# Kernel optimization log

Measured on AMD Instinct MI355X. Metric: run time of the kernel, lower is better.

## Reference

```python
import jax, jax.numpy as jnp
import numpy as np

MODEL_DIM = 256
NUM_HEADS = 4
HEAD_DIM = MODEL_DIM // NUM_HEADS
MAX_LEN = 512
EPS = 1e-5


def positional_embedding(n, dim):
    pos = jnp.arange(n, dtype=jnp.float32)[:, None]
    div = jnp.exp(jnp.arange(0, dim, 2, dtype=jnp.float32) * (-np.log(10000.0) / dim))
    pe = jnp.zeros((n, dim), dtype=jnp.float32)
    pe = pe.at[:, 0::2].set(jnp.sin(pos * div))
    pe = pe.at[:, 1::2].set(jnp.cos(pos * div))
    return pe


def layer_norm(x, g, b):
    mu = jnp.mean(x, axis=-1, keepdims=True)
    var = jnp.mean(jnp.square(x - mu), axis=-1, keepdims=True)
    return (x - mu) * jax.lax.rsqrt(var + EPS) * g + b


def setup_inputs() -> dict:
    key = jax.random.key(0)
    ks = jax.random.split(key, 20)
    B, N = 64, 512
    d = MODEL_DIM

    def lin(k, fan_in, fan_out):
        lim = 1.0 / np.sqrt(fan_in)
        return jax.random.uniform(k, (fan_out, fan_in), jnp.float32, -lim, lim)

    def xavier(k, fan_in, fan_out):
        lim = np.sqrt(6.0 / (fan_in + fan_out))
        return jax.random.uniform(k, (fan_out, fan_in), jnp.float32, -lim, lim)

    return {
        "x": jax.random.normal(ks[0], (B, N, 769), jnp.float32),
        "y": jax.random.normal(ks[1], (B, N, 674), jnp.float32),
        "z": jnp.zeros((B, 1), jnp.float32),
        "Wr": lin(ks[2], 769, d), "br": jnp.zeros((d,), jnp.float32),
        "Wf": lin(ks[3], 674, d), "bf": jnp.zeros((d,), jnp.float32),
        "g_x": jnp.ones((d,), jnp.float32), "b_x": jnp.zeros((d,), jnp.float32),
        "g_y": jnp.ones((d,), jnp.float32), "b_y": jnp.zeros((d,), jnp.float32),
        "Wq": xavier(ks[4], d, d), "bq": jnp.zeros((d,), jnp.float32),
        "Wk": xavier(ks[5], d, d), "bk": jnp.zeros((d,), jnp.float32),
        "Wv": xavier(ks[6], d, d), "bv": jnp.zeros((d,), jnp.float32),
        "Wo": xavier(ks[7], d, d), "bo": jnp.zeros((d,), jnp.float32),
        "g_m": jnp.ones((d,), jnp.float32), "b_m": jnp.zeros((d,), jnp.float32),
        "W1": lin(ks[8], d, d), "b1": jnp.zeros((d,), jnp.float32),
        "W2": lin(ks[9], d, d), "b2": jnp.zeros((d,), jnp.float32),
        "Wc": lin(ks[10], d, 2), "bc": jnp.zeros((2,), jnp.float32),
    }


def reference(x, y, z, Wr, br, Wf, bf, g_x, b_x, g_y, b_y,
              Wq, bq, Wk, bk, Wv, bv, Wo, bo, g_m, b_m,
              W1, b1, W2, b2, Wc, bc):
    B, N, _ = x.shape
    d, H, hd = MODEL_DIM, NUM_HEADS, HEAD_DIM
    pe = positional_embedding(MAX_LEN, d)[:N]  # (N, d)

    xp = layer_norm(x @ Wr.T + br + pe[None], g_x, b_x)  # (B,N,d)
    yp = layer_norm(y @ Wf.T + bf + pe[None], g_y, b_y)

    # cross-attention (non-causal, no masks, eval-mode dropout)
    q = (xp @ Wq.T + bq).reshape(B, N, H, hd)
    k = (yp @ Wk.T + bk).reshape(B, N, H, hd)
    v = (yp @ Wv.T + bv).reshape(B, N, H, hd)
    scale = hd ** -0.5
    scores = jnp.einsum("bshd,bthd->bhst", q, k) * scale  # (B,H,N,N)
    attn = jax.nn.softmax(scores, axis=-1)
    ctx = jnp.einsum("bhst,bthd->bshd", attn, v).reshape(B, N, d)
    attn_out = ctx @ Wo.T + bo

    x_res = layer_norm(xp + attn_out, g_m, b_m)
    mlp = jax.nn.relu(x_res @ W1.T + b1) @ W2.T + b2
    x_mlp = x_res + mlp
    pooled = jnp.mean(x_mlp, axis=1)  # (B,d)
    logits = pooled @ Wc.T + bc  # (B,2)
    return logits
```

## Files before the change

kernel.cpp:

```cpp
#include <hip/hip_runtime.h>
#include <hip/hip_bf16.h>

#define B_   64
#define N_   512
#define D_   256
#define H_   4
#define HD_  64

typedef __hip_bfloat16 bf16;
typedef __attribute__((ext_vector_type(8))) short short8;
typedef __attribute__((ext_vector_type(4))) float floatx4;

__device__ __forceinline__ float bf2f(bf16 v) { return __bfloat162float(v); }
__device__ __forceinline__ unsigned short f2us(float f) {
    bf16 h = __float2bfloat16(f);
    union { bf16 h; unsigned short u; } c; c.h = h; return c.u;
}

typedef __attribute__((address_space(1))) const unsigned int asg_u32;
typedef __attribute__((address_space(3))) unsigned int asl_u32;
__device__ __forceinline__ void gl_lds16(const void* g, void* l) {
    __builtin_amdgcn_global_load_lds((asg_u32*)g, (asl_u32*)l, 16, 0, 0);
}

__device__ __forceinline__ void wait_vm12() { asm volatile("s_waitcnt vmcnt(12)" ::: "memory"); }
__device__ __forceinline__ void wait_vm5()  { asm volatile("s_waitcnt vmcnt(5)"  ::: "memory"); }
__device__ __forceinline__ void wait_vm0()  { asm volatile("s_waitcnt vmcnt(0)"  ::: "memory"); }
__device__ __forceinline__ void wait_lg0()  { asm volatile("s_waitcnt lgkmcnt(0)" ::: "memory"); }
__device__ __forceinline__ void bar()       { __builtin_amdgcn_s_barrier(); }
__device__ __forceinline__ void schedb()    { __builtin_amdgcn_sched_barrier(0); }

__global__ __launch_bounds__(256)
void convw_k(const float* __restrict__ Wr, const float* __restrict__ Wf,
             const float* __restrict__ Wq, const float* __restrict__ Wk,
             const float* __restrict__ Wv, const float* __restrict__ Wo,
             const float* __restrict__ W1, const float* __restrict__ W2,
             bf16* __restrict__ dst)
{
    const int seg = blockIdx.y;
    const float* src; int Kreal, Kp; size_t off;
    switch (seg) {
        case 0: src = Wr; Kreal = 769; Kp = 800; off = 0; break;
        case 1: src = Wf; Kreal = 674; Kp = 704; off = 256 * 800; break;
        default:
            src = (seg == 2) ? Wq : (seg == 3) ? Wk : (seg == 4) ? Wv
                : (seg == 5) ? Wo : (seg == 6) ? W1 : W2;
            Kreal = 256; Kp = 256;
            off = 256 * 800 + 256 * 704 + (size_t)(seg - 2) * 256 * 256;
            break;
    }
    const int idx = blockIdx.x * 256 + threadIdx.x;
    if (idx >= 256 * Kp / 8) return;
    const int rowk = idx * 8;
    const int n = rowk / Kp, k0 = rowk % Kp;
    unsigned short tmp[8];
    #pragma unroll
    for (int j = 0; j < 8; ++j) {
        int kk = k0 + j;
        tmp[j] = f2us(kk < Kreal ? src[(size_t)n * Kreal + kk] : 0.f);
    }
    *(short8*)&dst[off + (size_t)rowk] = *(short8*)tmp;
}

__global__ __launch_bounds__(256)
void pe_k(float* __restrict__ pe)
{
    const int n = blockIdx.x, c = threadIdx.x;
    const int j = c & ~1;
    float freq = __expf(-(float)j * (9.210340371976184f / 256.0f));
    float ang = (float)n * freq;
    pe[n * 256 + c] = (c & 1) ? cosf(ang) : sinf(ang);
}

template<bool F32A>
__global__ __launch_bounds__(256)
void gemm_rp_t(const bf16* __restrict__ A, const float* __restrict__ A32,
               int lda, int Kreal,
               const bf16* __restrict__ W, int ldw,
               const float* __restrict__ bias, const bf16* __restrict__ res,
               const float* __restrict__ pe,
               const float* __restrict__ g, const float* __restrict__ bln,
               bf16* __restrict__ C, float* __restrict__ pp,
               int Kp, int relu, int tv)
{
    __shared__ bf16 As[3][4 * 64 * 8];
    __shared__ bf16 Bs[3][4 * 256 * 8];
    __shared__ float s_mu[64][4], s_sq[64][4];

    const int tid = threadIdx.x;
    const int m0 = blockIdx.x * 64;
    const int lane = tid & 63, w = tid >> 6;
    const int fr = lane & 15, quad = lane >> 4;
    const int nt = Kp / 32;

    const unsigned short* Wp = (const unsigned short*)W + (size_t)lane * ldw + w * 8;

    floatx4 acc[4][4] = {};
    int rb = 0, w1 = 1, w2 = 2;

    if constexpr (F32A) {
        const int srow = tid >> 2, skb = tid & 3, kb8 = skb * 8;
        const float* a32p = A32 + (size_t)(m0 + srow) * Kreal + kb8;
        float avA[8], avB[8];

        #pragma unroll
        for (int j = 0; j < 8; ++j) avA[j] = a32p[j];
        #pragma unroll
        for (int i = 0; i < 4; ++i)
            gl_lds16(Wp + (size_t)(i * 64) * ldw, &Bs[0][(w * 256 + i * 64 + lane) * 8]);
        {
            unsigned short uw[8];
            #pragma unroll
            for (int j = 0; j < 8; ++j) uw[j] = f2us(avA[j]);
            *(short8*)&As[0][(skb * 64 + srow) * 8] = *(short8*)uw;
        }
        #pragma unroll
        for (int j = 0; j < 8; ++j) avB[j] = a32p[32 + j];
        #pragma unroll
        for (int i = 0; i < 4; ++i)
            gl_lds16(Wp + (size_t)(i * 64) * ldw + 32, &Bs[1][(w * 256 + i * 64 + lane) * 8]);

        auto f32a_step = [&](int t_, float (&AVC)[8], float (&AVN)[8]) {
            if (t_ + 1 < nt) { wait_vm12(); } else { wait_vm0(); }
            wait_lg0();
            bar();
            schedb();
            if (t_ + 2 < nt) {
                const int kL = (t_ + 2) * 32;
                if (kL + 32 <= Kreal) {
                    #pragma unroll
                    for (int j = 0; j < 8; ++j) AVN[j] = a32p[kL + j];
                } else {
                    #pragma unroll
                    for (int j = 0; j < 8; ++j) {
                        int kk = kL + kb8 + j;
                        int offv = (kk < Kreal) ? (kL + j) : 0;
                        float tvv = a32p[offv];
                        AVN[j] = (kk < Kreal) ? tvv : 0.f;
                    }
                }
                #pragma unroll
                for (int i = 0; i < 4; ++i)
                    gl_lds16(Wp + (size_t)(i * 64) * ldw + kL,
                             &Bs[w2][(w * 256 + i * 64 + lane) * 8]);
            }
            if (t_ + 1 < nt) {
                unsigned short uw[8];
                #pragma unroll
                for (int j = 0; j < 8; ++j) uw[j] = f2us(AVC[j]);
                *(short8*)&As[w1][(skb * 64 + srow) * 8] = *(short8*)uw;
            }
            schedb();
            short8 a[4];
            #pragma unroll
            for (int im = 0; im < 4; ++im)
                a[im] = *(const short8*)&As[rb][(quad * 64 + im * 16 + fr) * 8];
            #pragma unroll
            for (int in = 0; in < 4; ++in) {
                short8 bfrag = *(const short8*)&Bs[rb][(quad * 256 + w * 64 + in * 16 + fr) * 8];
                #pragma unroll
                for (int im = 0; im < 4; ++im)
                    acc[im][in] = __builtin_amdgcn_mfma_f32_16x16x32_bf16(
                        a[im], bfrag, acc[im][in], 0, 0, 0);
            }
            int tmp_ = rb; rb = w1; w1 = w2; w2 = tmp_;
        };
        for (int t = 0; t < nt; t += 2) {
            f32a_step(t, avB, avA);
            if (t + 1 < nt) f32a_step(t + 1, avA, avB);
        }
    } else {
        const unsigned short* Ap = (const unsigned short*)A + (size_t)(m0 + lane) * lda + w * 8;

        gl_lds16(Ap, &As[0][(w * 64 + lane) * 8]);
        #pragma unroll
        for (int i = 0; i < 4; ++i)
            gl_lds16(Wp + (size_t)(i * 64) * ldw, &Bs[0][(w * 256 + i * 64 + lane) * 8]);
        gl_lds16(Ap + 32, &As[1][(w * 64 + lane) * 8]);
        #pragma unroll
        for (int i = 0; i < 4; ++i)
            gl_lds16(Wp + (size_t)(i * 64) * ldw + 32, &Bs[1][(w * 256 + i * 64 + lane) * 8]);

        for (int t = 0; t < nt; ++t) {
            if (t + 1 < nt) { wait_vm5(); } else { wait_vm0(); }
            bar();
            schedb();
            if (t + 2 < nt) {
                const int kB = (t + 2) * 32;
                gl_lds16(Ap + kB, &As[w2][(w * 64 + lane) * 8]);
                #pragma unroll
                for (int i = 0; i < 4; ++i)
                    gl_lds16(Wp + (size_t)(i * 64) * ldw + kB,
                             &Bs[w2][(w * 256 + i * 64 + lane) * 8]);
            }
            schedb();
            short8 a[4];
            #pragma unroll
            for (int im = 0; im < 4; ++im)
                a[im] = *(const short8*)&As[rb][(quad * 64 + im * 16 + fr) * 8];
            #pragma unroll
            for (int in = 0; in < 4; ++in) {
                short8 bfrag = *(const short8*)&Bs[rb][(quad * 256 + w * 64 + in * 16 + fr) * 8];
                #pragma unroll
                for (int im = 0; im < 4; ++im)
                    acc[im][in] = __builtin_amdgcn_mfma_f32_16x16x32_bf16(
                        a[im], bfrag, acc[im][in], 0, 0, 0);
            }
            int tmp_ = rb; rb = w1; w1 = w2; w2 = tmp_;
        }
    }

    #pragma unroll
    for (int in = 0; in < 4; ++in) {
        const int n = w * 64 + in * 16 + fr;
        const float bi = bias[n];
        #pragma unroll
        for (int im = 0; im < 4; ++im) {
            #pragma unroll
            for (int reg = 0; reg < 4; ++reg) {
                const int m = m0 + im * 16 + quad * 4 + reg;
                float v = acc[im][in][reg] + bi;
                if (pe)   v += pe[((m & (N_ - 1)) << 8) + n];
                if (relu) v = fmaxf(v, 0.f);
                if (res)  v += bf2f(res[((size_t)m << 8) + n]);
                acc[im][in][reg] = v;
            }
        }
    }

    if (g) {
        #pragma unroll
        for (int im = 0; im < 4; ++im) {
            #pragma unroll
            for (int reg = 0; reg < 4; ++reg) {
                float ps = acc[im][0][reg] + acc[im][1][reg]
                         + acc[im][2][reg] + acc[im][3][reg];
                float pq = acc[im][0][reg] * acc[im][0][reg]
                         + acc[im][1][reg] * acc[im][1][reg]
                         + acc[im][2][reg] * acc[im][2][reg]
                         + acc[im][3][reg] * acc[im][3][reg];
                #pragma unroll
                for (int off = 1; off < 16; off <<= 1) {
                    ps += __shfl_xor(ps, off, 64);
                    pq += __shfl_xor(pq, off, 64);
                }
                if (fr == 0) {
                    const int r = im * 16 + quad * 4 + reg;
                    s_mu[r][w] = ps;
                    s_sq[r][w] = pq;
                }
            }
        }
        __syncthreads();
        #pragma unroll
        for (int im = 0; im < 4; ++im) {
            #pragma unroll
            for (int reg = 0; reg < 4; ++reg) {
                const int r = im * 16 + quad * 4 + reg;
                const float mu = (s_mu[r][0] + s_mu[r][1] + s_mu[r][2] + s_mu[r][3])
                                 * (1.f / 256.f);
                const float var = (s_sq[r][0] + s_sq[r][1] + s_sq[r][2] + s_sq[r][3])
                                  * (1.f / 256.f) - mu * mu;
                const float rs = rsqrtf(var + 1e-5f);
                const int m = m0 + r;
                #pragma unroll
                for (int in = 0; in < 4; ++in) {
                    const int n = w * 64 + in * 16 + fr;
                    C[((size_t)m << 8) + n] = __float2bfloat16(
                        (acc[im][in][reg] - mu) * rs * g[n] + bln[n]);
                }
            }
        }
    } else if (tv) {
        const int bh = ((m0 >> 9) << 2) + w;
        const int nn = m0 & (N_ - 1);
        unsigned short* Ct = (unsigned short*)C;
        #pragma unroll
        for (int in = 0; in < 4; ++in) {
            const int d = in * 16 + fr;
            #pragma unroll
            for (int im = 0; im < 4; ++im) {
                unsigned short pk[4];
                #pragma unroll
                for (int reg = 0; reg < 4; ++reg) pk[reg] = f2us(acc[im][in][reg]);
                *(ushort4*)&Ct[((size_t)(bh * 64 + d) << 9) + nn + im * 16 + quad * 4]
                    = *(ushort4*)pk;
            }
        }
    } else {
        #pragma unroll
        for (int im = 0; im < 4; ++im) {
            #pragma unroll
            for (int reg = 0; reg < 4; ++reg) {
                const int m = m0 + im * 16 + quad * 4 + reg;
                #pragma unroll
                for (int in = 0; in < 4; ++in) {
                    const int n = w * 64 + in * 16 + fr;
                    C[((size_t)m << 8) + n] = __float2bfloat16(acc[im][in][reg]);
                }
            }
        }
        if (pp) {
            #pragma unroll
            for (int in = 0; in < 4; ++in) {
                float s = 0.f;
                #pragma unroll
                for (int im = 0; im < 4; ++im)
                    #pragma unroll
                    for (int reg = 0; reg < 4; ++reg) s += acc[im][in][reg];
                s += __shfl_xor(s, 16, 64);
                s += __shfl_xor(s, 32, 64);
                if (quad == 0)
                    pp[((m0 >> 6) << 8) + w * 64 + in * 16 + fr] = s;
            }
        }
    }
}

__global__ __launch_bounds__(256)
void attn_k(const bf16* q, const bf16* __restrict__ k,
            const bf16* __restrict__ vt, bf16* ctx)
{
    __shared__ bf16 Ks[8 * 64 * 8];
    __shared__ bf16 Vs[8 * 64 * 8];
    __shared__ bf16 Ps[4 * 16 * 72];

    const int bid = blockIdx.x;
    const int l = (bid & 7) * 256 + (bid >> 3);
    const int qt = l & 7;
    const int h  = (l >> 3) & 3;
    const int b  = l >> 5;
    const int q0 = qt * 64;
    const size_t base  = ((size_t)b * N_) * D_ + h * HD_;
    const size_t vbase = ((size_t)(b * H_ + h) * HD_) * N_;

    const int tid = threadIdx.x;
    const int lane = tid & 63;
    const int w = tid >> 6;
    const int fr = lane & 15, quad = lane >> 4;

    short8 aq[2];
    #pragma unroll
    for (int ks = 0; ks < 2; ++ks)
        aq[ks] = *(const short8*)((const unsigned short*)q + base
                   + (size_t)(q0 + w * 16 + fr) * D_ + (ks * 4 + quad) * 8);

    floatx4 O[4] = {};
    float mrun[4], lrun[4];
    #pragma unroll
    for (int r = 0; r < 4; ++r) { mrun[r] = -1e30f; lrun[r] = 0.f; }

    const int srow = tid >> 2, sc = tid & 3;
    const unsigned short* kp = (const unsigned short*)k + base + (size_t)srow * D_ + sc * 16;
    const unsigned short* vp = (const unsigned short*)vt + vbase + (size_t)srow * N_ + sc * 16;
    const float C1 = 0.125f * 1.44269504f;

    for (int kt = 0; kt < 8; ++kt) {
        __syncthreads();
        {
            const unsigned short* srck = kp + (size_t)(kt * 64) * D_;
            *(short8*)&Ks[((sc * 2 + 0) * 64 + srow) * 8] = *(const short8*)(srck);
            *(short8*)&Ks[((sc * 2 + 1) * 64 + srow) * 8] = *(const short8*)(srck + 8);
            const unsigned short* srcv = vp + kt * 64;
            *(short8*)&Vs[((sc * 2 + 0) * 64 + srow) * 8] = *(const short8*)(srcv);
            *(short8*)&Vs[((sc * 2 + 1) * 64 + srow) * 8] = *(const short8*)(srcv + 8);
        }
        __syncthreads();

        floatx4 S[4] = {};
        __builtin_amdgcn_s_setprio(1);
        #pragma unroll
        for (int in = 0; in < 4; ++in) {
            #pragma unroll
            for (int ks = 0; ks < 2; ++ks) {
                short8 bk = *(const short8*)&Ks[((ks * 4 + quad) * 64 + in * 16 + fr) * 8];
                S[in] = __builtin_amdgcn_mfma_f32_16x16x32_bf16(aq[ks], bk, S[in], 0, 0, 0);
            }
        }
        __builtin_amdgcn_s_setprio(0);

        #pragma unroll
        for (int r = 0; r < 4; ++r) {
            float mloc = fmaxf(fmaxf(S[0][r], S[1][r]), fmaxf(S[2][r], S[3][r]));
            #pragma unroll
            for (int off = 1; off < 16; off <<= 1) mloc = fmaxf(mloc, __shfl_xor(mloc, off, 64));
            float mnew = fmaxf(mrun[r], mloc);
            float mc = mnew * C1;
            float alpha = exp2f(mrun[r] * C1 - mc);
            float rs = 0.f;
            #pragma unroll
            for (int in = 0; in < 4; ++in) {
                float p = exp2f(S[in][r] * C1 - mc);
                S[in][r] = p;
                rs += p;
            }
            #pragma unroll
            for (int off = 1; off < 16; off <<= 1) rs += __shfl_xor(rs, off, 64);
            lrun[r] = lrun[r] * alpha + rs;
            mrun[r] = mnew;
            #pragma unroll
            for (int in = 0; in < 4; ++in) O[in][r] *= alpha;
        }

        #pragma unroll
        for (int in = 0; in < 4; ++in)
            #pragma unroll
            for (int r = 0; r < 4; ++r)
                Ps[(w * 16 + quad * 4 + r) * 72 + in * 16 + fr] = __float2bfloat16(S[in][r]);
        short8 pa[2];
        #pragma unroll
        for (int ks = 0; ks < 2; ++ks)
            pa[ks] = *(const short8*)&Ps[(w * 16 + fr) * 72 + ks * 32 + quad * 8];

        __builtin_amdgcn_s_setprio(1);
        #pragma unroll
        for (int in = 0; in < 4; ++in) {
            #pragma unroll
            for (int ks = 0; ks < 2; ++ks) {
                short8 bv = *(const short8*)&Vs[((ks * 4 + quad) * 64 + in * 16 + fr) * 8];
                O[in] = __builtin_amdgcn_mfma_f32_16x16x32_bf16(pa[ks], bv, O[in], 0, 0, 0);
            }
        }
        __builtin_amdgcn_s_setprio(0);
    }

    #pragma unroll
    for (int r = 0; r < 4; ++r) {
        const float inv = 1.f / lrun[r];
        const int row = q0 + w * 16 + quad * 4 + r;
        #pragma unroll
        for (int in = 0; in < 4; ++in)
            ctx[base + (size_t)row * D_ + in * 16 + fr] = __float2bfloat16(O[in][r] * inv);
    }
}

__global__ __launch_bounds__(256)
void logits_k(const float* __restrict__ partial, const float* __restrict__ Wc,
              const float* __restrict__ bc, float* __restrict__ out)
{
    __shared__ float pl[256];
    __shared__ float red[256];
    int b = blockIdx.x, c = threadIdx.x;
    float s = 0.f;
    for (int ch = 0; ch < 8; ++ch) s += partial[((size_t)b * 8 + ch) * D_ + c];
    pl[c] = s * (1.f / 512.f);
    __syncthreads();
    int o = c >> 7, cc = c & 127;
    red[c] = pl[cc] * Wc[o * 256 + cc] + pl[cc + 128] * Wc[o * 256 + cc + 128];
    __syncthreads();
    for (int st = 64; st > 0; st >>= 1) { if (cc < st) red[c] += red[c + st]; __syncthreads(); }
    if (cc == 0) out[b * 2 + o] = red[c] + bc[o];
}

extern "C" void kernel_launch(void* const* d_in, const int* in_sizes, int n_in,
                              void* d_out, int out_size, void* d_ws, size_t ws_size,
                              hipStream_t stream)
{
    const float* x   = (const float*)d_in[0];
    const float* y   = (const float*)d_in[1];
    const float* Wr  = (const float*)d_in[3];
    const float* br  = (const float*)d_in[4];
    const float* Wf  = (const float*)d_in[5];
    const float* bfv = (const float*)d_in[6];
    const float* gx  = (const float*)d_in[7];
    const float* bx  = (const float*)d_in[8];
    const float* gy  = (const float*)d_in[9];
    const float* by  = (const float*)d_in[10];
    const float* Wq  = (const float*)d_in[11];
    const float* bq  = (const float*)d_in[12];
    const float* Wk  = (const float*)d_in[13];
    const float* bk  = (const float*)d_in[14];
    const float* Wv  = (const float*)d_in[15];
    const float* bv  = (const float*)d_in[16];
    const float* Wo  = (const float*)d_in[17];
    const float* bo  = (const float*)d_in[18];
    const float* gm  = (const float*)d_in[19];
    const float* bm  = (const float*)d_in[20];
    const float* W1  = (const float*)d_in[21];
    const float* b1  = (const float*)d_in[22];
    const float* W2  = (const float*)d_in[23];
    const float* b2  = (const float*)d_in[24];
    const float* Wc  = (const float*)d_in[25];
    const float* bc  = (const float*)d_in[26];

    bf16* ws = (bf16*)d_ws;
    const size_t S = (size_t)B_ * N_ * D_;
    bf16*  wb   = ws;
    float* pe   = (float*)(ws + 778240);
    float* part = pe + 131072;
    bf16*  bA   = ws + 778240 + 4 * 131072;
    bf16*  bB   = bA + S;
    bf16*  bC   = bB + S;
    bf16*  bD   = bC + S;
    bf16*  bE   = bD + S;

    bf16* Wrb = wb;
    bf16* Wfb = wb + 256 * 800;
    bf16* Wqb = Wfb + 256 * 704;
    bf16* Wkb = Wqb + 65536;
    bf16* Wvb = Wkb + 65536;
    bf16* Wob = Wvb + 65536;
    bf16* W1b = Wob + 65536;
    bf16* W2b = W1b + 65536;

    const int M = B_ * N_;
    dim3 blk(256);
    dim3 grp(M / 64);

    pe_k<<<N_, blk, 0, stream>>>(pe);
    convw_k<<<dim3(100, 8), blk, 0, stream>>>(Wr, Wf, Wq, Wk, Wv, Wo, W1, W2, wb);

    gemm_rp_t<true><<<grp, blk, 0, stream>>>(nullptr, x, 0, 769, Wrb, 800,
        br, nullptr, pe, gx, bx, bA, nullptr, 800, 0, 0);
    gemm_rp_t<true><<<grp, blk, 0, stream>>>(nullptr, y, 0, 674, Wfb, 704,
        bfv, nullptr, pe, gy, by, bB, nullptr, 704, 0, 0);
    gemm_rp_t<false><<<grp, blk, 0, stream>>>(bA, nullptr, 256, 256, Wqb, 256,
        bq, nullptr, nullptr, nullptr, nullptr, bC, nullptr, 256, 0, 0);
    gemm_rp_t<false><<<grp, blk, 0, stream>>>(bB, nullptr, 256, 256, Wkb, 256,
        bk, nullptr, nullptr, nullptr, nullptr, bD, nullptr, 256, 0, 0);
    gemm_rp_t<false><<<grp, blk, 0, stream>>>(bB, nullptr, 256, 256, Wvb, 256,
        bv, nullptr, nullptr, nullptr, nullptr, bE, nullptr, 256, 0, 1);
    attn_k<<<B_ * H_ * 8, blk, 0, stream>>>(bC, bD, bE, bC);
    gemm_rp_t<false><<<grp, blk, 0, stream>>>(bC, nullptr, 256, 256, Wob, 256,
        bo, bA, nullptr, gm, bm, bD, nullptr, 256, 0, 0);
    gemm_rp_t<false><<<grp, blk, 0, stream>>>(bD, nullptr, 256, 256, W1b, 256,
        b1, nullptr, nullptr, nullptr, nullptr, bE, nullptr, 256, 1, 0);
    gemm_rp_t<false><<<grp, blk, 0, stream>>>(bE, nullptr, 256, 256, W2b, 256,
        b2, bD, nullptr, nullptr, nullptr, bB, part, 256, 0, 0);
    logits_k<<<B_, blk, 0, stream>>>(part, Wc, bc, (float*)d_out);
}
```

Baseline: 549.9 us.

## Fuse K/V projections into one kernel and W1/W2 MLP into one kernel

```diff
diff --git a/kernel.cpp b/kernel.cpp
--- a/kernel.cpp
+++ b/kernel.cpp
@@ -271,22 +271,6 @@
                 }
             }
         }
-    } else if (tv) {
-        const int bh = ((m0 >> 9) << 2) + w;
-        const int nn = m0 & (N_ - 1);
-        unsigned short* Ct = (unsigned short*)C;
-        #pragma unroll
-        for (int in = 0; in < 4; ++in) {
-            const int d = in * 16 + fr;
-            #pragma unroll
-            for (int im = 0; im < 4; ++im) {
-                unsigned short pk[4];
-                #pragma unroll
-                for (int reg = 0; reg < 4; ++reg) pk[reg] = f2us(acc[im][in][reg]);
-                *(ushort4*)&Ct[((size_t)(bh * 64 + d) << 9) + nn + im * 16 + quad * 4]
-                    = *(ushort4*)pk;
-            }
-        }
     } else {
         #pragma unroll
         for (int im = 0; im < 4; ++im) {
@@ -300,19 +284,187 @@
                 }
             }
         }
-        if (pp) {
-            #pragma unroll
-            for (int in = 0; in < 4; ++in) {
-                float s = 0.f;
+    }
+}
+
+__global__ __launch_bounds__(512, 4)
+void kv_k(const bf16* __restrict__ A,
+          const bf16* __restrict__ Wk, const bf16* __restrict__ Wv,
+          const float* __restrict__ bk, const float* __restrict__ bv,
+          bf16* __restrict__ K, bf16* __restrict__ Vt)
+{
+    const int tid = threadIdx.x;
+    const int m0 = blockIdx.x * 64;
+    const int lane = tid & 63, w = tid >> 6;
+    const int isv = w >> 2;
+    const int cq = w & 3;
+    const int fr = lane & 15, quad = lane >> 4;
+
+    const unsigned short* wp = (const unsigned short*)(isv ? Wv : Wk)
+        + (size_t)(cq * 64 + fr) * 256 + quad * 8;
+    const unsigned short* ap = (const unsigned short*)A
+        + (size_t)(m0 + fr) * 256 + quad * 8;
+
+    floatx4 acc[4][4] = {};
+    for (int t = 0; t < 8; ++t) {
+        const int k0 = t * 32;
+        short8 fa[4], fb[4];
+        #pragma unroll
+        for (int i = 0; i < 4; ++i) {
+            fa[i] = *(const short8*)(ap + (size_t)(i * 16) * 256 + k0);
+            fb[i] = *(const short8*)(wp + (size_t)(i * 16) * 256 + k0);
+        }
+        #pragma unroll
+        for (int in = 0; in < 4; ++in)
+            #pragma unroll
+            for (int im = 0; im < 4; ++im)
+                acc[im][in] = __builtin_amdgcn_mfma_f32_16x16x32_bf16(
+                    fa[im], fb[in], acc[im][in], 0, 0, 0);
+    }
+
+    const float* bias = isv ? bv : bk;
+    if (!isv) {
+        #pragma unroll
+        for (int im = 0; im < 4; ++im) {
+            #pragma unroll
+            for (int reg = 0; reg < 4; ++reg) {
+                const int m = m0 + im * 16 + quad * 4 + reg;
+                #pragma unroll
+                for (int in = 0; in < 4; ++in) {
+                    const int n = cq * 64 + in * 16 + fr;
+                    K[((size_t)m << 8) + n] = __float2bfloat16(acc[im][in][reg] + bias[n]);
+                }
+            }
+        }
+    } else {
+        const int bh = ((m0 >> 9) << 2) + cq;
+        const int nn = m0 & (N_ - 1);
+        unsigned short* Ct = (unsigned short*)Vt;
+        #pragma unroll
+        for (int in = 0; in < 4; ++in) {
+            const int d = in * 16 + fr;
+            const float bi = bias[cq * 64 + d];
+            #pragma unroll
+            for (int im = 0; im < 4; ++im) {
+                unsigned short pk[4];
+                #pragma unroll
+                for (int reg = 0; reg < 4; ++reg) pk[reg] = f2us(acc[im][in][reg] + bi);
+                *(ushort4*)&Ct[((size_t)(bh * 64 + d) << 9) + nn + im * 16 + quad * 4]
+                    = *(ushort4*)pk;
+            }
+        }
+    }
+}
+
+__global__ __launch_bounds__(256)
+void mlp_k(const bf16* __restrict__ A,
+           const bf16* __restrict__ W1, const float* __restrict__ b1,
+           const bf16* __restrict__ W2, const float* __restrict__ b2,
+           bf16* __restrict__ C, float* __restrict__ pp)
+{
+    __shared__ bf16 Hs[64 * 256];
+
+    const int tid = threadIdx.x;
+    const int m0 = blockIdx.x * 64;
+    const int lane = tid & 63, cq = tid >> 6;
+    const int fr = lane & 15, quad = lane >> 4;
+
+    const unsigned short* ap  = (const unsigned short*)A  + (size_t)(m0 + fr) * 256 + quad * 8;
+    const unsigned short* w1p = (const unsigned short*)W1 + (size_t)(cq * 64 + fr) * 256 + quad * 8;
+
+    {
+        floatx4 acc[4][4] = {};
+        for (int t = 0; t < 8; ++t) {
+            const int k0 = t * 32;
+            short8 fa[4], fb[4];
+            #pragma unroll
+            for (int i = 0; i < 4; ++i) {
+                fa[i] = *(const short8*)(ap + (size_t)(i * 16) * 256 + k0);
+                fb[i] = *(const short8*)(w1p + (size_t)(i * 16) * 256 + k0);
+            }
+            #pragma unroll
+            for (int in = 0; in < 4; ++in)
                 #pragma unroll
                 for (int im = 0; im < 4; ++im)
-                    #pragma unroll
-                    for (int reg = 0; reg < 4; ++reg) s += acc[im][in][reg];
-                s += __shfl_xor(s, 16, 64);
-                s += __shfl_xor(s, 32, 64);
-                if (quad == 0)
-                    pp[((m0 >> 6) << 8) + w * 64 + in * 16 + fr] = s;
-            }
+                    acc[im][in] = __builtin_amdgcn_mfma_f32_16x16x32_bf16(
+                        fa[im], fb[in], acc[im][in], 0, 0, 0);
+        }
+        #pragma unroll
+        for (int in = 0; in < 4; ++in) {
+            const int col = cq * 64 + in * 16 + fr;
+            const float bi = b1[col];
+            #pragma unroll
+            for (int im = 0; im < 4; ++im) {
+                #pragma unroll
+                for (int reg = 0; reg < 4; ++reg) {
+                    const int row = im * 16 + quad * 4 + reg;
+                    const int idx = row * 256 + col;
+                    Hs[idx ^ ((row & 7) << 3)] =
+                        __float2bfloat16(fmaxf(acc[im][in][reg] + bi, 0.f));
+                }
+            }
+        }
+    }
+    __syncthreads();
+
+    floatx4 acc2[4][4] = {};
+    const unsigned short* w2p = (const unsigned short*)W2 + (size_t)(cq * 64 + fr) * 256 + quad * 8;
+    for (int t = 0; t < 8; ++t) {
+        const int k0 = t * 32;
+        short8 fa[4], fb[4];
+        #pragma unroll
+        for (int i = 0; i < 4; ++i) {
+            fa[i] = *(const short8*)(w2p + (size_t)(i * 16) * 256 + k0);
+            const int hrow = i * 16 + fr;
+            const int idx = hrow * 256 + k0 + quad * 8;
+            fb[i] = *(const short8*)&Hs[idx ^ ((hrow & 7) << 3)];
+        }
+        #pragma unroll
+        for (int in = 0; in < 4; ++in)
+            #pragma unroll
+            for (int im = 0; im < 4; ++im)
+                acc2[im][in] = __builtin_amdgcn_mfma_f32_16x16x32_bf16(
+                    fa[im], fb[in], acc2[im][in], 0, 0, 0);
+    }
+
+    float ps[4][4];
+    #pragma unroll
+    for (int im = 0; im < 4; ++im)
+        #pragma unroll
+        for (int reg = 0; reg < 4; ++reg) ps[im][reg] = 0.f;
+
+    #pragma unroll
+    for (int im = 0; im < 4; ++im) {
+        #pragma unroll
+        for (int in = 0; in < 4; ++in) {
+            const int m = m0 + in * 16 + fr;
+            const int n2b = cq * 64 + im * 16 + quad * 4;
+            const ushort4 rv = *(const ushort4*)((const unsigned short*)A
+                                                 + ((size_t)m << 8) + n2b);
+            const unsigned short ru[4] = { rv.x, rv.y, rv.z, rv.w };
+            unsigned short pk[4];
+            #pragma unroll
+            for (int reg = 0; reg < 4; ++reg) {
+                bf16 rb_;
+                union { unsigned short u; bf16 h; } cvu; cvu.u = ru[reg]; rb_ = cvu.h;
+                float v = acc2[im][in][reg] + b2[n2b + reg] + bf2f(rb_);
+                ps[im][reg] += v;
+                pk[reg] = f2us(v);
+            }
+            *(ushort4*)((unsigned short*)C + ((size_t)m << 8) + n2b) = *(ushort4*)pk;
+        }
+    }
+    #pragma unroll
+    for (int im = 0; im < 4; ++im) {
+        #pragma unroll
+        for (int reg = 0; reg < 4; ++reg) {
+            float s = ps[im][reg];
+            s += __shfl_xor(s, 1, 64);
+            s += __shfl_xor(s, 2, 64);
+            s += __shfl_xor(s, 4, 64);
+            s += __shfl_xor(s, 8, 64);
+            if (fr == 0)
+                pp[(size_t)blockIdx.x * 256 + cq * 64 + im * 16 + quad * 4 + reg] = s;
         }
     }
 }
@@ -505,6 +657,7 @@
 
     const int M = B_ * N_;
     dim3 blk(256);
+    dim3 blk512(512);
     dim3 grp(M / 64);
 
     pe_k<<<N_, blk, 0, stream>>>(pe);
@@ -516,16 +669,10 @@
         bfv, nullptr, pe, gy, by, bB, nullptr, 704, 0, 0);
     gemm_rp_t<false><<<grp, blk, 0, stream>>>(bA, nullptr, 256, 256, Wqb, 256,
         bq, nullptr, nullptr, nullptr, nullptr, bC, nullptr, 256, 0, 0);
-    gemm_rp_t<false><<<grp, blk, 0, stream>>>(bB, nullptr, 256, 256, Wkb, 256,
-        bk, nullptr, nullptr, nullptr, nullptr, bD, nullptr, 256, 0, 0);
-    gemm_rp_t<false><<<grp, blk, 0, stream>>>(bB, nullptr, 256, 256, Wvb, 256,
-        bv, nullptr, nullptr, nullptr, nullptr, bE, nullptr, 256, 0, 1);
+    kv_k<<<grp, blk512, 0, stream>>>(bB, Wkb, Wvb, bk, bv, bD, bE);
     attn_k<<<B_ * H_ * 8, blk, 0, stream>>>(bC, bD, bE, bC);
     gemm_rp_t<false><<<grp, blk, 0, stream>>>(bC, nullptr, 256, 256, Wob, 256,
         bo, bA, nullptr, gm, bm, bD, nullptr, 256, 0, 0);
-    gemm_rp_t<false><<<grp, blk, 0, stream>>>(bD, nullptr, 256, 256, W1b, 256,
-        b1, nullptr, nullptr, nullptr, nullptr, bE, nullptr, 256, 1, 0);
-    gemm_rp_t<false><<<grp, blk, 0, stream>>>(bE, nullptr, 256, 256, W2b, 256,
-        b2, bD, nullptr, nullptr, nullptr, bB, part, 256, 0, 0);
+    mlp_k<<<grp, blk, 0, stream>>>(bD, W1b, b1, W2b, b2, bB, part);
     logits_k<<<B_, blk, 0, stream>>>(part, Wc, bc, (float*)d_out);
 }
```

Result: faster. 527.4 us (-4.1%).
